# Optimization experiments

Measured on AMD Instinct MI355X. Metric: run time of the kernel, lower is better.

Reference implementation:

```python
import jax, jax.numpy as jnp
import numpy as np

B, S, D = 16, 300, 768   # batch, hubert frames, embedding_dim
K = 512                  # vq codebook size
V = 5000                 # vocab size
H = 8                    # attention heads
NL = 4                   # encoder/decoder layers
L = 50                   # label length
EPS = 1e-5


def layer_norm(x, g, b):
    m = jnp.mean(x, axis=-1, keepdims=True)
    v = jnp.var(x, axis=-1, keepdims=True)
    return (x - m) * jax.lax.rsqrt(v + EPS) * g + b


def mha(q_in, kv_in, Wqkv, bqkv, Wo, bo, bias=None):
    # PyTorch nn.MultiheadAttention math (packed in_proj), batch_first
    Dm = q_in.shape[-1]
    hd = Dm // H
    Wq, Wk, Wv = jnp.split(Wqkv, 3, axis=0)
    bq, bk, bv = jnp.split(bqkv, 3, axis=0)
    q = (q_in @ Wq.T + bq).reshape(q_in.shape[0], -1, H, hd)
    k = (kv_in @ Wk.T + bk).reshape(kv_in.shape[0], -1, H, hd)
    v = (kv_in @ Wv.T + bv).reshape(kv_in.shape[0], -1, H, hd)
    scores = jnp.einsum('bthd,bshd->bhts', q, k) / jnp.sqrt(jnp.float32(hd))
    if bias is not None:
        scores = scores + bias
    a = jax.nn.softmax(scores, axis=-1)
    o = jnp.einsum('bhts,bshd->bthd', a, v).reshape(q_in.shape[0], -1, Dm)
    return o @ Wo.T + bo


def setup_inputs() -> dict:
    key = jax.random.key(0)
    ks = iter(jax.random.split(key, 64))
    f32 = jnp.float32
    def rn(shape, s=0.02):
        return jax.random.normal(next(ks), shape, f32) * s
    d = {}
    d['features'] = jax.random.normal(next(ks), (B, S, D), f32)
    d['labels'] = jax.random.randint(next(ks), (B, L), 1, V, jnp.int32)
    d['codebook'] = jax.random.normal(next(ks), (K, D), f32)   # normal_() init
    d['emb_layer'] = jax.random.normal(next(ks), (K, D), f32)  # nn.Embedding N(0,1)
    d['tok_emb'] = jax.random.normal(next(ks), (V, D), f32)
    d['fc_W'] = rn((V, D)); d['fc_b'] = jnp.zeros((V,), f32)
    for p in ['enc', 'dec_s', 'dec_c']:
        d[p + 'Wqkv' if p != 'enc' else 'enc_Wqkv'] = rn((NL, 3 * D, D))
    # rebuild cleanly with explicit names
    d['enc_Wqkv'] = rn((NL, 3 * D, D)); d['enc_bqkv'] = jnp.zeros((NL, 3 * D), f32)
    d['enc_Wo'] = rn((NL, D, D)); d['enc_bo'] = jnp.zeros((NL, D), f32)
    d['enc_ln1g'] = jnp.ones((NL, D), f32); d['enc_ln1b'] = jnp.zeros((NL, D), f32)
    d['enc_W1'] = rn((NL, 1536, D)); d['enc_b1'] = jnp.zeros((NL, 1536), f32)
    d['enc_W2'] = rn((NL, D, 1536)); d['enc_b2'] = jnp.zeros((NL, D), f32)
    d['enc_ln2g'] = jnp.ones((NL, D), f32); d['enc_ln2b'] = jnp.zeros((NL, D), f32)
    d['dec_sWqkv'] = rn((NL, 3 * D, D)); d['dec_sbqkv'] = jnp.zeros((NL, 3 * D), f32)
    d['dec_sWo'] = rn((NL, D, D)); d['dec_sbo'] = jnp.zeros((NL, D), f32)
    d['dec_cWqkv'] = rn((NL, 3 * D, D)); d['dec_cbqkv'] = jnp.zeros((NL, 3 * D), f32)
    d['dec_cWo'] = rn((NL, D, D)); d['dec_cbo'] = jnp.zeros((NL, D), f32)
    d['dec_ln1g'] = jnp.ones((NL, D), f32); d['dec_ln1b'] = jnp.zeros((NL, D), f32)
    d['dec_ln2g'] = jnp.ones((NL, D), f32); d['dec_ln2b'] = jnp.zeros((NL, D), f32)
    d['dec_ln3g'] = jnp.ones((NL, D), f32); d['dec_ln3b'] = jnp.zeros((NL, D), f32)
    d['dec_W1'] = rn((NL, 1536, D)); d['dec_b1'] = jnp.zeros((NL, 1536), f32)
    d['dec_W2'] = rn((NL, D, 1536)); d['dec_b2'] = jnp.zeros((NL, D), f32)
    return d


def forward(features, labels, codebook, emb_layer, tok_emb, fc_W, fc_b,
            enc_Wqkv, enc_bqkv, enc_Wo, enc_bo, enc_ln1g, enc_ln1b,
            enc_W1, enc_b1, enc_W2, enc_b2, enc_ln2g, enc_ln2b,
            dec_sWqkv, dec_sbqkv, dec_sWo, dec_sbo,
            dec_cWqkv, dec_cbqkv, dec_cWo, dec_cbo,
            dec_ln1g, dec_ln1b, dec_ln2g, dec_ln2b, dec_ln3g, dec_ln3b,
            dec_W1, dec_b1, dec_W2, dec_b2):
    # ---- VQ: pairwise distances + argmin + codebook gather ----
    x = features.reshape(-1, D)                                  # [N, D]
    dist = (jnp.sum(x * x, 1, keepdims=True)
            + jnp.sum(codebook * codebook, 1)
            - 2.0 * x @ codebook.T)                              # [N, K]
    idx = jnp.argmin(dist, axis=1)                               # [N]
    quantized = codebook[idx]                                    # one-hot @ codebook == gather
    # commitment loss (quantized is detached in e_latent_loss)
    vq_loss = 0.25 * jnp.mean((jax.lax.stop_gradient(quantized) - x) ** 2)
    # ---- encoder over embedding_layer lookup of the VQ indices ----
    h = emb_layer[idx].reshape(B, S, D)
    for i in range(NL):
        h = layer_norm(h + mha(h, h, enc_Wqkv[i], enc_bqkv[i], enc_Wo[i], enc_bo[i]),
                       enc_ln1g[i], enc_ln1b[i])
        ff = jax.nn.relu(h @ enc_W1[i].T + enc_b1[i]) @ enc_W2[i].T + enc_b2[i]
        h = layer_norm(h + ff, enc_ln2g[i], enc_ln2b[i])
    memory = h
    # ---- decoder (teacher forcing) ----
    dec_in = tok_emb[labels][:, :-1, :]                          # [B, L-1, D]
    target = labels[:, 1:]                                       # [B, L-1]
    T = L - 1
    causal = jnp.triu(jnp.ones((T, T), bool), 1)                 # tgt_mask
    kpm = (target == 0)[:, None, None, :]                        # tgt_key_padding_mask
    bias = jnp.where(causal[None, None] | kpm, jnp.float32(-1e9), jnp.float32(0.0))
    y = dec_in
    for i in range(NL):
        y = layer_norm(y + mha(y, y, dec_sWqkv[i], dec_sbqkv[i], dec_sWo[i], dec_sbo[i], bias),
                       dec_ln1g[i], dec_ln1b[i])
        y = layer_norm(y + mha(y, memory, dec_cWqkv[i], dec_cbqkv[i], dec_cWo[i], dec_cbo[i]),
                       dec_ln2g[i], dec_ln2b[i])
        ff = jax.nn.relu(y @ dec_W1[i].T + dec_b1[i]) @ dec_W2[i].T + dec_b2[i]
        y = layer_norm(y + ff, dec_ln3g[i], dec_ln3b[i])
    logits = y @ fc_W.T + fc_b                                   # [B, L-1, V]
    return logits, vq_loss, target


def reference(features, labels, codebook, emb_layer, tok_emb, fc_W, fc_b,
              enc_Wqkv, enc_bqkv, enc_Wo, enc_bo, enc_ln1g, enc_ln1b,
              enc_W1, enc_b1, enc_W2, enc_b2, enc_ln2g, enc_ln2b,
              dec_sWqkv, dec_sbqkv, dec_sWo, dec_sbo,
              dec_cWqkv, dec_cbqkv, dec_cWo, dec_cbo,
              dec_ln1g, dec_ln1b, dec_ln2g, dec_ln2b, dec_ln3g, dec_ln3b,
              dec_W1, dec_b1, dec_W2, dec_b2):
    return forward(features, labels, codebook, emb_layer, tok_emb, fc_W, fc_b,
                   enc_Wqkv, enc_bqkv, enc_Wo, enc_bo, enc_ln1g, enc_ln1b,
                   enc_W1, enc_b1, enc_W2, enc_b2, enc_ln2g, enc_ln2b,
                   dec_sWqkv, dec_sbqkv, dec_sWo, dec_sbo,
                   dec_cWqkv, dec_cbqkv, dec_cWo, dec_cbo,
                   dec_ln1g, dec_ln1b, dec_ln2g, dec_ln2b, dec_ln3g, dec_ln3b,
                   dec_W1, dec_b1, dec_W2, dec_b2)
```

## Files before the change

kernel.cpp:

```cpp
#include <hip/hip_runtime.h>
#include <hip/hip_bf16.h>

#define Bz   16
#define Sz   300
#define Dz   768
#define Kc   512
#define Vz   5000
#define Hh   8
#define HD   96
#define Lz   50
#define Tz   49
#define NTOK 4800
#define NDTOK 784

typedef short bf16x8 __attribute__((ext_vector_type(8)));
typedef float f32x4  __attribute__((ext_vector_type(4)));
typedef unsigned short us8 __attribute__((ext_vector_type(8)));

__device__ __forceinline__ unsigned short f2b(float f) {
    unsigned u = __float_as_uint(f);
    unsigned r = (u + 0x7fffu + ((u >> 16) & 1u)) >> 16;
    return (unsigned short)r;
}
__device__ __forceinline__ float b2f(unsigned short h) {
    return __uint_as_float(((unsigned)h) << 16);
}

__device__ __forceinline__ void glds16(const unsigned short* g, unsigned short* l) {
    __builtin_amdgcn_global_load_lds(
        (const __attribute__((address_space(1))) void*)g,
        (__attribute__((address_space(3))) void*)l, 16, 0, 0);
}

__global__ __launch_bounds__(256) void gemm_bf16_kernel(
    const unsigned short* __restrict__ A,
    const unsigned short* __restrict__ Bw,
    float* __restrict__ Cf,
    unsigned short* __restrict__ Cb,
    int ldc,
    const float* __restrict__ bias,
    const float* __restrict__ resid, int ldr,
    int relu, int M, int N, int Kd)
{
    __shared__ unsigned short As[128 * 32];
    __shared__ unsigned short Bs[128 * 32];
    const int tid  = threadIdx.x;
    const int wave = tid >> 6, lane = tid & 63;
    const int row0 = blockIdx.y * 128, col0 = blockIdx.x * 128;

    const int c0 = wave * 2;
    const int srow = lane >> 2;
    const int skcol = (lane & 3) * 8;
    int rA0 = row0 + c0 * 16 + srow;        if (rA0 > M - 1) rA0 = M - 1;
    int rA1 = row0 + (c0 + 1) * 16 + srow;  if (rA1 > M - 1) rA1 = M - 1;
    int rB0 = col0 + c0 * 16 + srow;        if (rB0 > N - 1) rB0 = N - 1;
    int rB1 = col0 + (c0 + 1) * 16 + srow;  if (rB1 > N - 1) rB1 = N - 1;
    const unsigned short* pA0 = A + (size_t)rA0 * Kd + skcol;
    const unsigned short* pA1 = A + (size_t)rA1 * Kd + skcol;
    const unsigned short* pB0 = Bw + (size_t)rB0 * Kd + skcol;
    const unsigned short* pB1 = Bw + (size_t)rB1 * Kd + skcol;
    unsigned short* lA0 = &As[c0 * 512];
    unsigned short* lA1 = &As[(c0 + 1) * 512];
    unsigned short* lB0 = &Bs[c0 * 512];
    unsigned short* lB1 = &Bs[(c0 + 1) * 512];

    const int wr = (wave >> 1) * 64, wc = (wave & 1) * 64;
    const int fr = lane & 15;
    const int kq = (lane >> 4) * 8;

    f32x4 acc[4][4];
    const f32x4 zero = { 0.f, 0.f, 0.f, 0.f };
#pragma unroll
    for (int i = 0; i < 4; ++i)
#pragma unroll
        for (int j = 0; j < 4; ++j) acc[i][j] = zero;

    for (int k0 = 0; k0 < Kd; k0 += 32) {
        __syncthreads();
        glds16(pA0 + k0, lA0);
        glds16(pA1 + k0, lA1);
        glds16(pB0 + k0, lB0);
        glds16(pB1 + k0, lB1);
        __syncthreads();

        bf16x8 af[4], bfr[4];
#pragma unroll
        for (int i = 0; i < 4; ++i)
            af[i] = *(const bf16x8*)(const void*)(&As[(wr + i * 16 + fr) * 32 + kq]);
#pragma unroll
        for (int j = 0; j < 4; ++j)
            bfr[j] = *(const bf16x8*)(const void*)(&Bs[(wc + j * 16 + fr) * 32 + kq]);
#pragma unroll
        for (int i = 0; i < 4; ++i)
#pragma unroll
            for (int j = 0; j < 4; ++j)
                acc[i][j] = __builtin_amdgcn_mfma_f32_16x16x32_bf16(
                    af[i], bfr[j], acc[i][j], 0, 0, 0);
    }

    const int rbase = row0 + wr + ((lane >> 4) << 2);
    const int cbase = col0 + wc + (lane & 15);
#pragma unroll
    for (int i = 0; i < 4; ++i) {
#pragma unroll
        for (int r = 0; r < 4; ++r) {
            int row = rbase + i * 16 + r;
            if (row >= M) continue;
#pragma unroll
            for (int j = 0; j < 4; ++j) {
                int col = cbase + j * 16;
                if (col >= N) continue;
                float v = acc[i][j][r];
                if (bias)  v += bias[col];
                if (resid) v += resid[(size_t)row * ldr + col];
                if (relu)  v = fmaxf(v, 0.f);
                if (Cf) Cf[(size_t)row * ldc + col] = v;
                if (Cb) Cb[(size_t)row * ldc + col] = f2b(v);
            }
        }
    }
}

__global__ __launch_bounds__(256) void gemm_bf16_32_kernel(
    const unsigned short* __restrict__ A,
    const unsigned short* __restrict__ Bw,
    float* __restrict__ Cf, unsigned short* __restrict__ Cb, int ldc,
    const float* __restrict__ bias,
    const float* __restrict__ resid, int ldr,
    int relu, int M, int N, int Kd)
{
    __shared__ unsigned short As[32 * 32];
    __shared__ unsigned short Bs[64 * 32];
    const int tid = threadIdx.x, wave = tid >> 6, lane = tid & 63;
    const int row0 = blockIdx.y * 32, col0 = blockIdx.x * 64;
    const int fr = lane & 15, quad = lane >> 4;
    const int sr = lane >> 2;
    const int sc = (lane & 3) * 8;

    const unsigned short* pA = nullptr;
    const unsigned short* pB0 = nullptr;
    const unsigned short* pB1 = nullptr;
    unsigned short* lA = nullptr;
    unsigned short* lB0 = nullptr;
    unsigned short* lB1 = nullptr;
    if (wave < 2) {
        int ra = row0 + wave * 16 + sr; if (ra > M - 1) ra = M - 1;
        pA = A + (size_t)ra * Kd + sc;
        lA = &As[wave * 512];
    } else {
        int w2 = wave - 2;
        int rb0 = col0 + w2 * 16 + sr;       if (rb0 > N - 1) rb0 = N - 1;
        int rb1 = col0 + 32 + w2 * 16 + sr;  if (rb1 > N - 1) rb1 = N - 1;
        pB0 = Bw + (size_t)rb0 * Kd + sc;
        pB1 = Bw + (size_t)rb1 * Kd + sc;
        lB0 = &Bs[w2 * 512];
        lB1 = &Bs[1024 + w2 * 512];
    }

    f32x4 acc[2];
    acc[0] = (f32x4){ 0.f, 0.f, 0.f, 0.f };
    acc[1] = (f32x4){ 0.f, 0.f, 0.f, 0.f };

    const int mrow = (wave & 1) * 16 + fr;
    const int ng = (wave >> 1) * 32;

    for (int k0 = 0; k0 < Kd; k0 += 32) {
        __syncthreads();
        if (wave < 2) {
            glds16(pA + k0, lA);
        } else {
            glds16(pB0 + k0, lB0);
            glds16(pB1 + k0, lB1);
        }
        __syncthreads();
        bf16x8 a = *(const bf16x8*)(const void*)(&As[mrow * 32 + quad * 8]);
#pragma unroll
        for (int t = 0; t < 2; ++t) {
            bf16x8 b = *(const bf16x8*)(const void*)(&Bs[(ng + t * 16 + fr) * 32 + quad * 8]);
            acc[t] = __builtin_amdgcn_mfma_f32_16x16x32_bf16(a, b, acc[t], 0, 0, 0);
        }
    }

    const int rbase = row0 + (wave & 1) * 16 + quad * 4;
    const int cbase = col0 + ng + fr;
#pragma unroll
    for (int r = 0; r < 4; ++r) {
        int row = rbase + r;
        if (row >= M) continue;
#pragma unroll
        for (int t = 0; t < 2; ++t) {
            int col = cbase + t * 16;
            if (col >= N) continue;
            float v = acc[t][r];
            if (bias)  v += bias[col];
            if (resid) v += resid[(size_t)row * ldr + col];
            if (relu)  v = fmaxf(v, 0.f);
            if (Cf) Cf[(size_t)row * ldc + col] = v;
            if (Cb) Cb[(size_t)row * ldc + col] = f2b(v);
        }
    }
}

__global__ __launch_bounds__(256) void vq_split_kernel(
    const float* __restrict__ src, unsigned short* __restrict__ dst,
    int nrows, int pattern)
{
    int i = blockIdx.x * 256 + threadIdx.x;
    if (i >= nrows * Dz) return;
    int r = i / Dz, c = i % Dz;
    float x = src[i];
    unsigned short h = f2b(x);
    unsigned short l = f2b(x - b2f(h));
    unsigned short* d = dst + (size_t)r * 2304 + c;
    if (pattern == 0) { d[0] = h; d[768] = h; d[1536] = l; }
    else              { d[0] = h; d[768] = l; d[1536] = h; }
}

#define SC_LD 324
#define P_LD  328
#define QK_LD 104
#define VT_LD 40

__global__ __launch_bounds__(256) void attn_mfma_kernel(
    const unsigned short* __restrict__ Qp, int qld, int qoff,
    const unsigned short* __restrict__ Kp, int kld, int koff,
    const unsigned short* __restrict__ Vp, int vld, int voff,
    unsigned short* __restrict__ Op,
    int Sq, int Sk, float scale, int causal,
    const int* __restrict__ lab)
{
    const int qt = blockIdx.x, h = blockIdx.y, b = blockIdx.z;
    const int q0 = qt * 32;
    __shared__ __align__(16) unsigned short Qs[32 * QK_LD];
    __shared__ __align__(16) unsigned short KVu[96 * VT_LD];
    __shared__ __align__(16) float Sc[32 * SC_LD];
    __shared__ __align__(16) unsigned short Pb[32 * P_LD];
    __shared__ float rinv[32];

    const int tid = threadIdx.x;
    const int wave = tid >> 6, lane = tid & 63;
    const int fr = lane & 15, quad = lane >> 4;
    const int nst = (Sk + 31) / 32;
    const int cmax = nst * 32;

    for (int e = tid; e < 384; e += 256) {
        int r = e / 12, c8 = (e % 12) * 8;
        int gq = q0 + r; if (gq >= Sq) gq = Sq - 1;
        us8 v = *(const us8*)(Qp + (size_t)(b * Sq + gq) * qld + qoff + h * HD + c8);
        *(us8*)(&Qs[r * QK_LD + c8]) = v;
    }

    const int mi = wave & 1;
    const int sw = wave >> 1;
    for (int it = 0; it < nst; ++it) {
        int s0 = it * 32;
        __syncthreads();
        for (int e = tid; e < 384; e += 256) {
            int r = e / 12, c8 = (e % 12) * 8;
            int gk = s0 + r; if (gk >= Sk) gk = Sk - 1;
            us8 v = *(const us8*)(Kp + (size_t)(b * Sk + gk) * kld + koff + h * HD + c8);
            *(us8*)(&KVu[r * QK_LD + c8]) = v;
        }
        __syncthreads();
        f32x4 acc = { 0.f, 0.f, 0.f, 0.f };
#pragma unroll
        for (int kk = 0; kk < 3; ++kk) {
            bf16x8 a = *(const bf16x8*)(const void*)(&Qs[(mi * 16 + fr) * QK_LD + kk * 32 + quad * 8]);
            bf16x8 bb = *(const bf16x8*)(const void*)(&KVu[(sw * 16 + fr) * QK_LD + kk * 32 + quad * 8]);
            acc = __builtin_amdgcn_mfma_f32_16x16x32_bf16(a, bb, acc, 0, 0, 0);
        }
        float* dst = &Sc[(mi * 16 + quad * 4) * SC_LD + s0 + sw * 16 + fr];
#pragma unroll
        for (int r = 0; r < 4; ++r) dst[r * SC_LD] = acc[r];
    }
    __syncthreads();

    {
        const int r = tid >> 3, sub = tid & 7;
        const int gq = q0 + r;
        float mx = -3e38f;
        for (int c = sub; c < cmax; c += 8) {
            float v = Sc[r * SC_LD + c];
            bool ok = (c < Sk);
            if (causal && c > gq) ok = false;
            if (ok && lab && lab[b * Lz + c + 1] == 0) ok = false;
            v = ok ? v * scale : -3e38f;
            Sc[r * SC_LD + c] = v;
            mx = fmaxf(mx, v);
        }
#pragma unroll
        for (int off = 4; off > 0; off >>= 1) mx = fmaxf(mx, __shfl_xor(mx, off));
        float sum = 0.f;
        for (int c = sub; c < cmax; c += 8) {
            float p = __expf(Sc[r * SC_LD + c] - mx);
            sum += p;
            Pb[r * P_LD + c] = f2b(p);
        }
#pragma unroll
        for (int off = 4; off > 0; off >>= 1) sum += __shfl_xor(sum, off);
        if (sub == 0) rinv[r] = 1.f / sum;
    }

    const int nbase = (wave >> 1) * 3;
    f32x4 oacc[3];
#pragma unroll
    for (int t = 0; t < 3; ++t) oacc[t] = (f32x4){ 0.f, 0.f, 0.f, 0.f };

    for (int it = 0; it < nst; ++it) {
        int s0 = it * 32;
        __syncthreads();
        for (int e = tid; e < 384; e += 256) {
            int r = e / 12, c8 = (e % 12) * 8;
            int gk = s0 + r; if (gk >= Sk) gk = Sk - 1;
            us8 v = *(const us8*)(Vp + (size_t)(b * Sk + gk) * vld + voff + h * HD + c8);
            const int f = ((c8 >> 3) & 3) << 3;
            const int rx = r ^ f;
#pragma unroll
            for (int j = 0; j < 8; ++j)
                KVu[(c8 + j) * VT_LD + rx] = v[j];
        }
        __syncthreads();
        bf16x8 a = *(const bf16x8*)(const void*)(&Pb[(mi * 16 + fr) * P_LD + s0 + quad * 8]);
#pragma unroll
        for (int t = 0; t < 3; ++t) {
            const int dcol = (nbase + t) * 16 + fr;
            const int f2 = ((dcol >> 3) & 3) << 3;
            bf16x8 bv = *(const bf16x8*)(const void*)(&KVu[dcol * VT_LD + ((quad * 8) ^ f2)]);
            oacc[t] = __builtin_amdgcn_mfma_f32_16x16x32_bf16(a, bv, oacc[t], 0, 0, 0);
        }
    }

#pragma unroll
    for (int t = 0; t < 3; ++t) {
#pragma unroll
        for (int r = 0; r < 4; ++r) {
            int lrow = mi * 16 + quad * 4 + r;
            int grow = q0 + lrow;
            if (grow >= Sq) continue;
            int col = h * HD + (nbase + t) * 16 + fr;
            Op[(size_t)(b * Sq + grow) * Dz + col] = f2b(oacc[t][r] * rinv[lrow]);
        }
    }
}

__global__ __launch_bounds__(256) void ln_kernel(
    const float* __restrict__ X, float* __restrict__ Y,
    unsigned short* __restrict__ Ybf,
    const float* __restrict__ g, const float* __restrict__ bb)
{
    const int n = blockIdx.x;
    const int tid = threadIdx.x;
    const float* x = X + (size_t)n * Dz;
    float v0 = x[tid], v1 = x[tid + 256], v2 = x[tid + 512];
    float s = v0 + v1 + v2;
    float q = v0 * v0 + v1 * v1 + v2 * v2;
#pragma unroll
    for (int off = 32; off > 0; off >>= 1) {
        s += __shfl_down(s, off);
        q += __shfl_down(q, off);
    }
    __shared__ float sbuf[4], qbuf[4];
    __shared__ float mv[2];
    int wid = tid >> 6;
    if ((tid & 63) == 0) { sbuf[wid] = s; qbuf[wid] = q; }
    __syncthreads();
    if (tid == 0) {
        float ts = sbuf[0] + sbuf[1] + sbuf[2] + sbuf[3];
        float tq = qbuf[0] + qbuf[1] + qbuf[2] + qbuf[3];
        float mean = ts * (1.f / 768.f);
        float var = tq * (1.f / 768.f) - mean * mean;
        mv[0] = mean;
        mv[1] = rsqrtf(var + 1e-5f);
    }
    __syncthreads();
    float mean = mv[0], inv = mv[1];
    float* y = Y + (size_t)n * Dz;
    float r0 = (v0 - mean) * inv * g[tid]       + bb[tid];
    float r1 = (v1 - mean) * inv * g[tid + 256] + bb[tid + 256];
    float r2 = (v2 - mean) * inv * g[tid + 512] + bb[tid + 512];
    y[tid] = r0; y[tid + 256] = r1; y[tid + 512] = r2;
    if (Ybf) {
        unsigned short* yb = Ybf + (size_t)n * Dz;
        yb[tid] = f2b(r0); yb[tid + 256] = f2b(r1); yb[tid + 512] = f2b(r2);
    }
}

__global__ __launch_bounds__(256) void sumsq_kernel(
    const float* __restrict__ cb, float* __restrict__ out, float* __restrict__ loss)
{
    const int c = blockIdx.x, tid = threadIdx.x;
    if (c == 0 && tid == 0) *loss = 0.f;
    const float* x = cb + (size_t)c * Dz;
    float v0 = x[tid], v1 = x[tid + 256], v2 = x[tid + 512];
    float q = v0 * v0 + v1 * v1 + v2 * v2;
#pragma unroll
    for (int off = 32; off > 0; off >>= 1) q += __shfl_down(q, off);
    __shared__ float qbuf[4];
    int wid = tid >> 6;
    if ((tid & 63) == 0) qbuf[wid] = q;
    __syncthreads();
    if (tid == 0) out[c] = qbuf[0] + qbuf[1] + qbuf[2] + qbuf[3];
}

__global__ __launch_bounds__(256) void vq_post_kernel(
    const float* __restrict__ dots, const float* __restrict__ sumc2,
    const float* __restrict__ feats, const float* __restrict__ codebook,
    const float* __restrict__ emb, float* __restrict__ H,
    unsigned short* __restrict__ Hbf,
    float* __restrict__ loss)
{
    const int n = blockIdx.x, tid = threadIdx.x;
    float best = 3.4e38f; int bi = 0;
    for (int c = tid; c < Kc; c += 256) {
        float dct = sumc2[c] - 2.f * dots[(size_t)n * Kc + c];
        if (dct < best) { best = dct; bi = c; }
    }
#pragma unroll
    for (int off = 32; off > 0; off >>= 1) {
        float ov = __shfl_down(best, off);
        int   oi = __shfl_down(bi, off);
        if (ov < best || (ov == best && oi < bi)) { best = ov; bi = oi; }
    }
    __shared__ float vb[4]; __shared__ int ib[4];
    __shared__ int bidx;
    int wid = tid >> 6;
    if ((tid & 63) == 0) { vb[wid] = best; ib[wid] = bi; }
    __syncthreads();
    if (tid == 0) {
        float v = vb[0]; int i = ib[0];
        for (int w = 1; w < 4; ++w)
            if (vb[w] < v || (vb[w] == v && ib[w] < i)) { v = vb[w]; i = ib[w]; }
        bidx = i;
    }
    __syncthreads();
    const int c = bidx;
    float part = 0.f;
    for (int d = tid; d < Dz; d += 256) {
        float xv = feats[(size_t)n * Dz + d];
        float cv = codebook[(size_t)c * Dz + d];
        float df = cv - xv;
        part += df * df;
        float ev = emb[(size_t)c * Dz + d];
        H[(size_t)n * Dz + d] = ev;
        Hbf[(size_t)n * Dz + d] = f2b(ev);
    }
#pragma unroll
    for (int off = 32; off > 0; off >>= 1) part += __shfl_down(part, off);
    __shared__ float pb[4];
    if ((tid & 63) == 0) pb[wid] = part;
    __syncthreads();
    if (tid == 0) atomicAdd(loss, pb[0] + pb[1] + pb[2] + pb[3]);
}

__global__ __launch_bounds__(256) void dec_embed_kernel(
    const int* __restrict__ labels, const float* __restrict__ tok,
    float* __restrict__ Y, unsigned short* __restrict__ Ybf,
    float* __restrict__ tgt)
{
    const int t = blockIdx.x;
    const int b = t / Tz, pos = t % Tz;
    const int lab = labels[b * Lz + pos];
    const int tid = threadIdx.x;
    const float* src = tok + (size_t)lab * Dz;
    float* dst = Y + (size_t)t * Dz;
    unsigned short* dbf = Ybf + (size_t)t * Dz;
    float a = src[tid], b1 = src[tid + 256], c = src[tid + 512];
    dst[tid] = a; dst[tid + 256] = b1; dst[tid + 512] = c;
    dbf[tid] = f2b(a); dbf[tid + 256] = f2b(b1); dbf[tid + 512] = f2b(c);
    if (tid == 0) tgt[t] = (float)labels[b * Lz + pos + 1];
}

__global__ void finalize_kernel(const float* loss, float* out)
{
    out[0] = loss[0] * (0.25f / (float)(NTOK * Dz));
}

__global__ __launch_bounds__(256) void conv6_kernel(
    const float* p0, int n0, const float* p1, int n1,
    const float* p2, int n2, const float* p3, int n3,
    const float* p4, int n4, const float* p5, int n5,
    unsigned short* __restrict__ dst)
{
    const int m0 = n0 >> 2, m1 = n1 >> 2, m2 = n2 >> 2,
              m3 = n3 >> 2, m4 = n4 >> 2, m5 = n5 >> 2;
    const int total4 = m0 + m1 + m2 + m3 + m4 + m5;
    for (int i = blockIdx.x * blockDim.x + threadIdx.x; i < total4;
         i += gridDim.x * blockDim.x) {
        int j = i; const float* p;
        if (j < m0) { p = p0; }
        else { j -= m0;
            if (j < m1) { p = p1; }
            else { j -= m1;
                if (j < m2) { p = p2; }
                else { j -= m2;
                    if (j < m3) { p = p3; }
                    else { j -= m3;
                        if (j < m4) { p = p4; }
                        else { j -= m4; p = p5; }
                    }
                }
            }
        }
        float4 v = ((const float4*)p)[j];
        ushort4 o;
        o.x = f2b(v.x); o.y = f2b(v.y); o.z = f2b(v.z); o.w = f2b(v.w);
        ((ushort4*)dst)[i] = o;
    }
}

extern "C" void kernel_launch(void* const* d_in, const int* in_sizes, int n_in,
                              void* d_out, int out_size, void* d_ws, size_t ws_size,
                              hipStream_t stream)
{
    bool sig = (n_in > 8 && in_sizes[8] == 9216);
    int I_eWqkv, I_ebqkv, I_eWo, I_ebo, I_eln1g, I_eln1b, I_eW1, I_eb1, I_eW2, I_eb2,
        I_eln2g, I_eln2b, I_sWqkv, I_sbqkv, I_sWo, I_sbo, I_cWqkv, I_cbqkv, I_cWo,
        I_cbo, I_dln1g, I_dln1b, I_dln2g, I_dln2b, I_dln3g, I_dln3b, I_dW1, I_db1,
        I_dW2, I_db2;
    if (sig) {
        I_eWqkv = 7; I_ebqkv = 8; I_eWo = 9; I_ebo = 10; I_eln1g = 11; I_eln1b = 12;
        I_eW1 = 13; I_eb1 = 14; I_eW2 = 15; I_eb2 = 16; I_eln2g = 17; I_eln2b = 18;
        I_sWqkv = 19; I_sbqkv = 20; I_sWo = 21; I_sbo = 22;
        I_cWqkv = 23; I_cbqkv = 24; I_cWo = 25; I_cbo = 26;
        I_dln1g = 27; I_dln1b = 28; I_dln2g = 29; I_dln2b = 30; I_dln3g = 31; I_dln3b = 32;
        I_dW1 = 33; I_db1 = 34; I_dW2 = 35; I_db2 = 36;
    } else {
        I_eWqkv = 7; I_sWqkv = 8; I_cWqkv = 9;
        I_ebqkv = 10; I_eWo = 11; I_ebo = 12; I_eln1g = 13; I_eln1b = 14;
        I_eW1 = 15; I_eb1 = 16; I_eW2 = 17; I_eb2 = 18; I_eln2g = 19; I_eln2b = 20;
        I_sbqkv = 21; I_sWo = 22; I_sbo = 23;
        I_cbqkv = 24; I_cWo = 25; I_cbo = 26;
        I_dln1g = 27; I_dln1b = 28; I_dln2g = 29; I_dln2b = 30; I_dln3g = 31; I_dln3b = 32;
        I_dW1 = 33; I_db1 = 34; I_dW2 = 35; I_db2 = 36;
    }

    const float* feats = (const float*)d_in[0];
    const int*   labels = (const int*)d_in[1];
    const float* cb    = (const float*)d_in[2];
    const float* emb   = (const float*)d_in[3];
    const float* tok   = (const float*)d_in[4];
    const float* fcW   = (const float*)d_in[5];
    const float* fcb   = (const float*)d_in[6];
    const float* eWqkv = (const float*)d_in[I_eWqkv];
    const float* ebqkv = (const float*)d_in[I_ebqkv];
    const float* eWo   = (const float*)d_in[I_eWo];
    const float* ebo   = (const float*)d_in[I_ebo];
    const float* eln1g = (const float*)d_in[I_eln1g];
    const float* eln1b = (const float*)d_in[I_eln1b];
    const float* eW1   = (const float*)d_in[I_eW1];
    const float* eb1   = (const float*)d_in[I_eb1];
    const float* eW2   = (const float*)d_in[I_eW2];
    const float* eb2   = (const float*)d_in[I_eb2];
    const float* eln2g = (const float*)d_in[I_eln2g];
    const float* eln2b = (const float*)d_in[I_eln2b];
    const float* sWqkv = (const float*)d_in[I_sWqkv];
    const float* sbqkv = (const float*)d_in[I_sbqkv];
    const float* sWo   = (const float*)d_in[I_sWo];
    const float* sbo   = (const float*)d_in[I_sbo];
    const float* cWqkv = (const float*)d_in[I_cWqkv];
    const float* cbqkv = (const float*)d_in[I_cbqkv];
    const float* cWo   = (const float*)d_in[I_cWo];
    const float* cbo   = (const float*)d_in[I_cbo];
    const float* dln1g = (const float*)d_in[I_dln1g];
    const float* dln1b = (const float*)d_in[I_dln1b];
    const float* dln2g = (const float*)d_in[I_dln2g];
    const float* dln2b = (const float*)d_in[I_dln2b];
    const float* dln3g = (const float*)d_in[I_dln3g];
    const float* dln3b = (const float*)d_in[I_dln3b];
    const float* dW1   = (const float*)d_in[I_dW1];
    const float* db1   = (const float*)d_in[I_db1];
    const float* dW2   = (const float*)d_in[I_dW2];
    const float* db2   = (const float*)d_in[I_db2];

    float* ws    = (float*)d_ws;
    float* sumc2 = ws;
    float* loss  = ws + 512;
    float* Hb    = ws + 1024;
    float* T1    = ws + 3687424;
    float* dots  = ws + 7373824;
    float* Yb    = T1;
    float* T1d   = T1 + 602112;

    unsigned short* bfbase = (unsigned short*)(ws + 9831424);
    unsigned short* Hb_bf  = bfbase;
    unsigned short* ATT_bf = bfbase + 3686400;
    unsigned short* FF_bf  = bfbase + 7372800;
    unsigned short* Yb_bf  = bfbase + 14745600;
    unsigned short* Wbuf   = bfbase + 15347712;
    unsigned short* QKV_bf = bfbase + 22425600;
    unsigned short* QKVd_bf = QKV_bf;
    unsigned short* Qc_bf   = QKV_bf + 1806336;
    unsigned short* CKV_bf  = QKV_bf + 2408448;
    unsigned short* Asplit  = QKV_bf;
    unsigned short* Bsplit  = FF_bf;

    float* outF = (float*)d_out;

    auto gemmb = [&](const unsigned short* A, const unsigned short* W,
                     float* Cf, unsigned short* Cb, int ldc,
                     const float* bias, const float* resid, int ldr,
                     int relu, int M, int N, int Kd) {
        dim3 g((N + 127) / 128, (M + 127) / 128);
        gemm_bf16_kernel<<<g, 256, 0, stream>>>(A, W, Cf, Cb, ldc, bias, resid, ldr,
                                                relu, M, N, Kd);
    };
    auto gemmb32 = [&](const unsigned short* A, const unsigned short* W,
                       float* Cf, unsigned short* Cb, int ldc,
                       const float* bias, const float* resid, int ldr,
                       int relu, int M, int N, int Kd) {
        dim3 g((N + 63) / 64, (M + 31) / 32);
        gemm_bf16_32_kernel<<<g, 256, 0, stream>>>(A, W, Cf, Cb, ldc, bias, resid, ldr,
                                                   relu, M, N, Kd);
    };

    const float scale = 0.1020620726159658f;
    const float* Z = nullptr;

    sumsq_kernel<<<Kc, 256, 0, stream>>>(cb, sumc2, loss);
    vq_split_kernel<<<(NTOK * Dz + 255) / 256, 256, 0, stream>>>(feats, Asplit, NTOK, 0);
    vq_split_kernel<<<(Kc * Dz + 255) / 256, 256, 0, stream>>>(cb, Bsplit, Kc, 1);
    gemmb32(Asplit, Bsplit, dots, nullptr, Kc, Z, Z, 0, 0, NTOK, Kc, 2304);
    vq_post_kernel<<<NTOK, 256, 0, stream>>>(dots, sumc2, feats, cb, emb, Hb, Hb_bf, loss);
    finalize_kernel<<<1, 1, 0, stream>>>(loss, outF + 3920000);

    const int W_QKV = 2304 * 768, W_O = 768 * 768, W_F1 = 1536 * 768, W_F2 = 768 * 1536;
    for (int i = 0; i < 4; ++i) {
        conv6_kernel<<<2048, 256, 0, stream>>>(
            eWqkv + (size_t)i * W_QKV, W_QKV,
            eWo   + (size_t)i * W_O,   W_O,
            eW1   + (size_t)i * W_F1,  W_F1,
            eW2   + (size_t)i * W_F2,  W_F2,
            Z, 0, Z, 0, Wbuf);
        unsigned short* bWqkv = Wbuf;
        unsigned short* bWo   = Wbuf + W_QKV;
        unsigned short* bW1   = Wbuf + W_QKV + W_O;
        unsigned short* bW2   = Wbuf + W_QKV + W_O + W_F1;

        gemmb(Hb_bf, bWqkv, nullptr, QKV_bf, 2304, ebqkv + i * 2304, Z, 0, 0, NTOK, 2304, Dz);
        attn_mfma_kernel<<<dim3(10, Hh, Bz), 256, 0, stream>>>(
            QKV_bf, 2304, 0, QKV_bf, 2304, 768, QKV_bf, 2304, 1536, ATT_bf,
            Sz, Sz, scale, 0, nullptr);
        gemmb(ATT_bf, bWo, T1, nullptr, Dz, ebo + i * Dz, Hb, Dz, 0, NTOK, Dz, Dz);
        ln_kernel<<<NTOK, 256, 0, stream>>>(T1, Hb, Hb_bf, eln1g + i * Dz, eln1b + i * Dz);
        gemmb(Hb_bf, bW1, nullptr, FF_bf, 1536, eb1 + i * 1536, Z, 0, 1, NTOK, 1536, Dz);
        gemmb(FF_bf, bW2, T1, nullptr, Dz, eb2 + i * Dz, Hb, Dz, 0, NTOK, Dz, 1536);
        ln_kernel<<<NTOK, 256, 0, stream>>>(T1, Hb, Hb_bf, eln2g + i * Dz, eln2b + i * Dz);
    }

    dec_embed_kernel<<<NDTOK, 256, 0, stream>>>(labels, tok, Yb, Yb_bf, outF + 3920001);
    for (int i = 0; i < 4; ++i) {
        conv6_kernel<<<2048, 256, 0, stream>>>(
            sWqkv + (size_t)i * W_QKV, W_QKV,
            sWo   + (size_t)i * W_O,   W_O,
            cWqkv + (size_t)i * W_QKV, W_QKV,
            cWo   + (size_t)i * W_O,   W_O,
            dW1   + (size_t)i * W_F1,  W_F1,
            dW2   + (size_t)i * W_F2,  W_F2, Wbuf);
        unsigned short* bsWqkv = Wbuf;
        unsigned short* bsWo   = Wbuf + W_QKV;
        unsigned short* bcWqkv = Wbuf + W_QKV + W_O;
        unsigned short* bcWo   = Wbuf + 2 * W_QKV + W_O;
        unsigned short* bW1    = Wbuf + 2 * W_QKV + 2 * W_O;
        unsigned short* bW2    = Wbuf + 2 * W_QKV + 2 * W_O + W_F1;

        gemmb32(Yb_bf, bsWqkv, nullptr, QKVd_bf, 2304, sbqkv + i * 2304, Z, 0, 0, NDTOK, 2304, Dz);
        attn_mfma_kernel<<<dim3(2, Hh, Bz), 256, 0, stream>>>(
            QKVd_bf, 2304, 0, QKVd_bf, 2304, 768, QKVd_bf, 2304, 1536, ATT_bf,
            Tz, Tz, scale, 1, labels);
        gemmb32(ATT_bf, bsWo, T1d, nullptr, Dz, sbo + i * Dz, Yb, Dz, 0, NDTOK, Dz, Dz);
        ln_kernel<<<NDTOK, 256, 0, stream>>>(T1d, Yb, Yb_bf, dln1g + i * Dz, dln1b + i * Dz);
        gemmb32(Yb_bf, bcWqkv, nullptr, Qc_bf, Dz, cbqkv + i * 2304, Z, 0, 0, NDTOK, Dz, Dz);
        gemmb(Hb_bf, bcWqkv + (size_t)768 * 768, nullptr, CKV_bf, 1536,
              cbqkv + i * 2304 + 768, Z, 0, 0, NTOK, 1536, Dz);
        attn_mfma_kernel<<<dim3(2, Hh, Bz), 256, 0, stream>>>(
            Qc_bf, 768, 0, CKV_bf, 1536, 0, CKV_bf, 1536, 768, ATT_bf,
            Tz, Sz, scale, 0, nullptr);
        gemmb32(ATT_bf, bcWo, T1d, nullptr, Dz, cbo + i * Dz, Yb, Dz, 0, NDTOK, Dz, Dz);
        ln_kernel<<<NDTOK, 256, 0, stream>>>(T1d, Yb, Yb_bf, dln2g + i * Dz, dln2b + i * Dz);
        gemmb32(Yb_bf, bW1, nullptr, FF_bf, 1536, db1 + i * 1536, Z, 0, 1, NDTOK, 1536, Dz);
        gemmb32(FF_bf, bW2, T1d, nullptr, Dz, db2 + i * Dz, Yb, Dz, 0, NDTOK, Dz, 1536);
        ln_kernel<<<NDTOK, 256, 0, stream>>>(T1d, Yb, Yb_bf, dln3g + i * Dz, dln3b + i * Dz);
    }

    conv6_kernel<<<2048, 256, 0, stream>>>(fcW, Vz * Dz, Z, 0, Z, 0, Z, 0, Z, 0, Z, 0, Wbuf);
    gemmb32(Yb_bf, Wbuf, outF, nullptr, Vz, fcb, Z, 0, 0, NDTOK, Vz, Dz);
}
```

Measured before the change: 2.341 ms.

## Convert attention kernel to flash-style online softmax with 64-row query tiles

```diff
diff --git a/kernel.cpp b/kernel.cpp
--- a/kernel.cpp
+++ b/kernel.cpp
@@ -216,10 +216,10 @@
     else              { d[0] = h; d[768] = l; d[1536] = h; }
 }
 
-#define SC_LD 324
-#define P_LD  328
-#define QK_LD 104
+#define AQ_LD 104
+#define AK_LD 104
 #define VT_LD 40
+#define AP_LD 40
 
 __global__ __launch_bounds__(256) void attn_mfma_kernel(
     const unsigned short* __restrict__ Qp, int qld, int qoff,
@@ -230,115 +230,127 @@
     const int* __restrict__ lab)
 {
     const int qt = blockIdx.x, h = blockIdx.y, b = blockIdx.z;
-    const int q0 = qt * 32;
-    __shared__ __align__(16) unsigned short Qs[32 * QK_LD];
-    __shared__ __align__(16) unsigned short KVu[96 * VT_LD];
-    __shared__ __align__(16) float Sc[32 * SC_LD];
-    __shared__ __align__(16) unsigned short Pb[32 * P_LD];
-    __shared__ float rinv[32];
+    const int q0 = qt * 64;
+    __shared__ __align__(16) unsigned short Qs[64 * AQ_LD];
+    __shared__ __align__(16) unsigned short Ks[32 * AK_LD];
+    __shared__ __align__(16) unsigned short VT[96 * VT_LD];
+    __shared__ __align__(16) unsigned short Pb[64 * AP_LD];
 
     const int tid = threadIdx.x;
     const int wave = tid >> 6, lane = tid & 63;
     const int fr = lane & 15, quad = lane >> 4;
     const int nst = (Sk + 31) / 32;
-    const int cmax = nst * 32;
-
-    for (int e = tid; e < 384; e += 256) {
+
+    for (int e = tid; e < 768; e += 256) {
         int r = e / 12, c8 = (e % 12) * 8;
         int gq = q0 + r; if (gq >= Sq) gq = Sq - 1;
         us8 v = *(const us8*)(Qp + (size_t)(b * Sq + gq) * qld + qoff + h * HD + c8);
-        *(us8*)(&Qs[r * QK_LD + c8]) = v;
-    }
-
-    const int mi = wave & 1;
-    const int sw = wave >> 1;
+        *(us8*)(&Qs[r * AQ_LD + c8]) = v;
+    }
+
+    float mrow[4], lrow[4];
+#pragma unroll
+    for (int r = 0; r < 4; ++r) { mrow[r] = -3e38f; lrow[r] = 0.f; }
+    f32x4 oacc[6];
+#pragma unroll
+    for (int n = 0; n < 6; ++n) oacc[n] = (f32x4){ 0.f, 0.f, 0.f, 0.f };
+
+    const int lrow_base = wave * 16 + quad * 4;
+
     for (int it = 0; it < nst; ++it) {
-        int s0 = it * 32;
-        __syncthreads();
+        const int s0 = it * 32;
         for (int e = tid; e < 384; e += 256) {
             int r = e / 12, c8 = (e % 12) * 8;
             int gk = s0 + r; if (gk >= Sk) gk = Sk - 1;
-            us8 v = *(const us8*)(Kp + (size_t)(b * Sk + gk) * kld + koff + h * HD + c8);
-            *(us8*)(&KVu[r * QK_LD + c8]) = v;
-        }
-        __syncthreads();
-        f32x4 acc = { 0.f, 0.f, 0.f, 0.f };
-#pragma unroll
-        for (int kk = 0; kk < 3; ++kk) {
-            bf16x8 a = *(const bf16x8*)(const void*)(&Qs[(mi * 16 + fr) * QK_LD + kk * 32 + quad * 8]);
-            bf16x8 bb = *(const bf16x8*)(const void*)(&KVu[(sw * 16 + fr) * QK_LD + kk * 32 + quad * 8]);
-            acc = __builtin_amdgcn_mfma_f32_16x16x32_bf16(a, bb, acc, 0, 0, 0);
-        }
-        float* dst = &Sc[(mi * 16 + quad * 4) * SC_LD + s0 + sw * 16 + fr];
-#pragma unroll
-        for (int r = 0; r < 4; ++r) dst[r * SC_LD] = acc[r];
-    }
-    __syncthreads();
-
-    {
-        const int r = tid >> 3, sub = tid & 7;
-        const int gq = q0 + r;
-        float mx = -3e38f;
-        for (int c = sub; c < cmax; c += 8) {
-            float v = Sc[r * SC_LD + c];
-            bool ok = (c < Sk);
-            if (causal && c > gq) ok = false;
-            if (ok && lab && lab[b * Lz + c + 1] == 0) ok = false;
-            v = ok ? v * scale : -3e38f;
-            Sc[r * SC_LD + c] = v;
-            mx = fmaxf(mx, v);
-        }
-#pragma unroll
-        for (int off = 4; off > 0; off >>= 1) mx = fmaxf(mx, __shfl_xor(mx, off));
-        float sum = 0.f;
-        for (int c = sub; c < cmax; c += 8) {
-            float p = __expf(Sc[r * SC_LD + c] - mx);
-            sum += p;
-            Pb[r * P_LD + c] = f2b(p);
-        }
-#pragma unroll
-        for (int off = 4; off > 0; off >>= 1) sum += __shfl_xor(sum, off);
-        if (sub == 0) rinv[r] = 1.f / sum;
-    }
-
-    const int nbase = (wave >> 1) * 3;
-    f32x4 oacc[3];
-#pragma unroll
-    for (int t = 0; t < 3; ++t) oacc[t] = (f32x4){ 0.f, 0.f, 0.f, 0.f };
-
-    for (int it = 0; it < nst; ++it) {
-        int s0 = it * 32;
-        __syncthreads();
-        for (int e = tid; e < 384; e += 256) {
-            int r = e / 12, c8 = (e % 12) * 8;
-            int gk = s0 + r; if (gk >= Sk) gk = Sk - 1;
-            us8 v = *(const us8*)(Vp + (size_t)(b * Sk + gk) * vld + voff + h * HD + c8);
+            us8 kv = *(const us8*)(Kp + (size_t)(b * Sk + gk) * kld + koff + h * HD + c8);
+            *(us8*)(&Ks[r * AK_LD + c8]) = kv;
+            us8 vv = *(const us8*)(Vp + (size_t)(b * Sk + gk) * vld + voff + h * HD + c8);
             const int f = ((c8 >> 3) & 3) << 3;
             const int rx = r ^ f;
 #pragma unroll
             for (int j = 0; j < 8; ++j)
-                KVu[(c8 + j) * VT_LD + rx] = v[j];
+                VT[(c8 + j) * VT_LD + rx] = vv[j];
         }
         __syncthreads();
-        bf16x8 a = *(const bf16x8*)(const void*)(&Pb[(mi * 16 + fr) * P_LD + s0 + quad * 8]);
-#pragma unroll
-        for (int t = 0; t < 3; ++t) {
-            const int dcol = (nbase + t) * 16 + fr;
+
+        f32x4 sc[2];
+        sc[0] = (f32x4){ 0.f, 0.f, 0.f, 0.f };
+        sc[1] = (f32x4){ 0.f, 0.f, 0.f, 0.f };
+#pragma unroll
+        for (int kk = 0; kk < 3; ++kk) {
+            bf16x8 a = *(const bf16x8*)(const void*)(&Qs[(wave * 16 + fr) * AQ_LD + kk * 32 + quad * 8]);
+#pragma unroll
+            for (int t = 0; t < 2; ++t) {
+                bf16x8 bb = *(const bf16x8*)(const void*)(&Ks[(t * 16 + fr) * AK_LD + kk * 32 + quad * 8]);
+                sc[t] = __builtin_amdgcn_mfma_f32_16x16x32_bf16(a, bb, sc[t], 0, 0, 0);
+            }
+        }
+
+        bool cv[2];
+#pragma unroll
+        for (int t = 0; t < 2; ++t) {
+            int col = s0 + t * 16 + fr;
+            bool ok = (col < Sk);
+            if (ok && lab && lab[b * Lz + col + 1] == 0) ok = false;
+            cv[t] = ok;
+        }
+#pragma unroll
+        for (int r = 0; r < 4; ++r) {
+            int gq = q0 + lrow_base + r;
+#pragma unroll
+            for (int t = 0; t < 2; ++t) {
+                int col = s0 + t * 16 + fr;
+                bool ok = cv[t] && (!causal || col <= gq);
+                sc[t][r] = ok ? sc[t][r] * scale : -3e38f;
+            }
+        }
+
+        float p0[4], p1[4];
+#pragma unroll
+        for (int r = 0; r < 4; ++r) {
+            float mx = fmaxf(sc[0][r], sc[1][r]);
+#pragma unroll
+            for (int off = 1; off < 16; off <<= 1) mx = fmaxf(mx, __shfl_xor(mx, off));
+            float mnew = fmaxf(mrow[r], mx);
+            float alpha = __expf(mrow[r] - mnew);
+            float a0 = __expf(sc[0][r] - mnew);
+            float a1 = __expf(sc[1][r] - mnew);
+            float sum = a0 + a1;
+#pragma unroll
+            for (int off = 1; off < 16; off <<= 1) sum += __shfl_xor(sum, off);
+            lrow[r] = lrow[r] * alpha + sum;
+            mrow[r] = mnew;
+            p0[r] = a0; p1[r] = a1;
+#pragma unroll
+            for (int n = 0; n < 6; ++n) oacc[n][r] *= alpha;
+        }
+
+#pragma unroll
+        for (int r = 0; r < 4; ++r) {
+            Pb[(lrow_base + r) * AP_LD + fr]      = f2b(p0[r]);
+            Pb[(lrow_base + r) * AP_LD + 16 + fr] = f2b(p1[r]);
+        }
+
+        bf16x8 a = *(const bf16x8*)(const void*)(&Pb[(wave * 16 + fr) * AP_LD + quad * 8]);
+#pragma unroll
+        for (int n = 0; n < 6; ++n) {
+            const int dcol = n * 16 + fr;
             const int f2 = ((dcol >> 3) & 3) << 3;
-            bf16x8 bv = *(const bf16x8*)(const void*)(&KVu[dcol * VT_LD + ((quad * 8) ^ f2)]);
-            oacc[t] = __builtin_amdgcn_mfma_f32_16x16x32_bf16(a, bv, oacc[t], 0, 0, 0);
-        }
-    }
-
-#pragma unroll
-    for (int t = 0; t < 3; ++t) {
-#pragma unroll
-        for (int r = 0; r < 4; ++r) {
-            int lrow = mi * 16 + quad * 4 + r;
-            int grow = q0 + lrow;
-            if (grow >= Sq) continue;
-            int col = h * HD + (nbase + t) * 16 + fr;
-            Op[(size_t)(b * Sq + grow) * Dz + col] = f2b(oacc[t][r] * rinv[lrow]);
+            bf16x8 bv = *(const bf16x8*)(const void*)(&VT[dcol * VT_LD + ((quad * 8) ^ f2)]);
+            oacc[n] = __builtin_amdgcn_mfma_f32_16x16x32_bf16(a, bv, oacc[n], 0, 0, 0);
+        }
+        __syncthreads();
+    }
+
+#pragma unroll
+    for (int r = 0; r < 4; ++r) {
+        int grow = q0 + lrow_base + r;
+        if (grow >= Sq) continue;
+        float inv = 1.f / lrow[r];
+#pragma unroll
+        for (int n = 0; n < 6; ++n) {
+            int col = h * HD + n * 16 + fr;
+            Op[(size_t)(b * Sq + grow) * Dz + col] = f2b(oacc[n][r] * inv);
         }
     }
 }
@@ -637,7 +649,7 @@
         unsigned short* bW2   = Wbuf + W_QKV + W_O + W_F1;
 
         gemmb(Hb_bf, bWqkv, nullptr, QKV_bf, 2304, ebqkv + i * 2304, Z, 0, 0, NTOK, 2304, Dz);
-        attn_mfma_kernel<<<dim3(10, Hh, Bz), 256, 0, stream>>>(
+        attn_mfma_kernel<<<dim3(5, Hh, Bz), 256, 0, stream>>>(
             QKV_bf, 2304, 0, QKV_bf, 2304, 768, QKV_bf, 2304, 1536, ATT_bf,
             Sz, Sz, scale, 0, nullptr);
         gemmb(ATT_bf, bWo, T1, nullptr, Dz, ebo + i * Dz, Hb, Dz, 0, NTOK, Dz, Dz);
@@ -664,7 +676,7 @@
         unsigned short* bW2    = Wbuf + 2 * W_QKV + 2 * W_O + W_F1;
 
         gemmb32(Yb_bf, bsWqkv, nullptr, QKVd_bf, 2304, sbqkv + i * 2304, Z, 0, 0, NDTOK, 2304, Dz);
-        attn_mfma_kernel<<<dim3(2, Hh, Bz), 256, 0, stream>>>(
+        attn_mfma_kernel<<<dim3(1, Hh, Bz), 256, 0, stream>>>(
             QKVd_bf, 2304, 0, QKVd_bf, 2304, 768, QKVd_bf, 2304, 1536, ATT_bf,
             Tz, Tz, scale, 1, labels);
         gemmb32(ATT_bf, bsWo, T1d, nullptr, Dz, sbo + i * Dz, Yb, Dz, 0, NDTOK, Dz, Dz);
@@ -672,7 +684,7 @@
         gemmb32(Yb_bf, bcWqkv, nullptr, Qc_bf, Dz, cbqkv + i * 2304, Z, 0, 0, NDTOK, Dz, Dz);
         gemmb(Hb_bf, bcWqkv + (size_t)768 * 768, nullptr, CKV_bf, 1536,
               cbqkv + i * 2304 + 768, Z, 0, 0, NTOK, 1536, Dz);
-        attn_mfma_kernel<<<dim3(2, Hh, Bz), 256, 0, stream>>>(
+        attn_mfma_kernel<<<dim3(1, Hh, Bz), 256, 0, stream>>>(
             Qc_bf, 768, 0, CKV_bf, 1536, 0, CKV_bf, 1536, 768, ATT_bf,
             Tz, Sz, scale, 0, nullptr);
         gemmb32(ATT_bf, bcWo, T1d, nullptr, Dz, cbo + i * Dz, Yb, Dz, 0, NDTOK, Dz, Dz);
```

Result: faster. 2.145 ms (-8.4%).
